# Performance work log

Hardware: AMD Instinct MI355X
Metric: run time of the kernel (lower is better)

Reference implementation:

```python
import jax, jax.numpy as jnp
import numpy as np

R, K, H_IN, W_IN = 512, 17, 56, 56   # rois, keypoints, heatmap size
ROI_H = ROI_W = 96                   # = ceil(BOX_LEN), fixed by construction
BOX_LEN = 95.5                       # all boxes have this side length
A = -0.75                            # PyTorch bicubic coefficient


def _cubic(x):
    x = jnp.abs(x)
    near = ((A + 2.0) * x - (A + 3.0)) * x * x + 1.0
    far = A * (((x - 5.0) * x + 8.0) * x - 4.0)
    return jnp.where(x <= 1.0, near, jnp.where(x < 2.0, far, 0.0))


def _resize_matrix(out_size, in_size):
    """Dense [out,in] bicubic interpolation matrix (align_corners=False, border-replicate)."""
    scale = in_size / out_size
    src = (jnp.arange(out_size, dtype=jnp.float32) + 0.5) * scale - 0.5
    base = jnp.floor(src).astype(jnp.int32)
    taps = base[:, None] + jnp.arange(-1, 3)                      # [out, 4]
    w = _cubic(src[:, None] - taps.astype(jnp.float32))           # weights from unclamped dist
    taps = jnp.clip(taps, 0, in_size - 1)                         # replicate border
    rows = jnp.broadcast_to(jnp.arange(out_size)[:, None], taps.shape)
    return jnp.zeros((out_size, in_size), jnp.float32).at[rows, taps].add(w)


def setup_inputs() -> dict:
    key = jax.random.key(0)
    k1, k2 = jax.random.split(key)
    masks = jax.random.normal(k1, (R, K, H_IN, W_IN), dtype=jnp.float32)
    offs = jax.random.uniform(k2, (R, 2), jnp.float32, 0.0, 400.0)
    # corner format (c0_start, c1_start, c0_end, c1_end); all lengths == BOX_LEN
    boxes = jnp.concatenate([offs, offs + BOX_LEN], axis=1)
    return {"masks": masks, "boxes": boxes}


def reference(masks, boxes):
    My = _resize_matrix(ROI_H, H_IN)   # [ROI_H, H_IN]
    Mx = _resize_matrix(ROI_W, W_IN)   # [ROI_W, W_IN]
    # separable bicubic resize of every ROI heatmap: [R,K,ROI_H,ROI_W]
    roi = jnp.einsum('hi,rkij,wj->rkhw', My, masks, Mx)
    flat = roi.reshape(R, K, ROI_H * ROI_W)
    pos = jnp.argmax(flat, axis=-1)                                # [R,K]
    y = pos // ROI_W
    x = pos % ROI_W
    scores = jnp.take_along_axis(flat, pos[..., None], axis=-1)[..., 0]  # logit at argmax
    len0 = jnp.maximum(boxes[:, 2] - boxes[:, 0], 1.0)
    len1 = jnp.maximum(boxes[:, 3] - boxes[:, 1], 1.0)
    corr0 = (len0 / ROI_H)[:, None]
    corr1 = (len1 / ROI_W)[:, None]
    p0 = (y.astype(jnp.float32) + 0.5) * corr0 + boxes[:, 0:1]
    p1 = (x.astype(jnp.float32) + 0.5) * corr1 + boxes[:, 1:2]
    predictions = jnp.stack([p0, p1, jnp.ones_like(p0)], axis=1)   # [R, n_dim+1, K]
    return predictions, scores
```

## Files before the change

### kernel.cpp

```cpp
#include <hip/hip_runtime.h>

#define R_    512
#define K_    17
#define HIN   56
#define WIN   56
#define OUTS  96
#define NMAP  (R_ * K_)
#define NT    192
#define TS    98
#define TROWS 32

typedef float v2f __attribute__((ext_vector_type(2)));

constexpr float cubic_c(float xin) {
    float x = xin < 0.0f ? -xin : xin;
    const float A = -0.75f;
    if (x <= 1.0f) return ((A + 2.0f) * x - (A + 3.0f)) * x * x + 1.0f;
    if (x < 2.0f)  return A * (((x - 5.0f) * x + 8.0f) * x - 4.0f);
    return 0.0f;
}

struct XTabT {
    float w[OUTS][4];
    int   s[OUTS];
    constexpr XTabT() : w{}, s{} {
        for (int o = 0; o < OUTS; ++o) {
            float src = ((float)o + 0.5f) * (56.0f / 96.0f) - 0.5f;
            int base = (int)src;
            if ((float)base > src) --base;
            int st = base - 1;
            if (st < 0) st = 0;
            if (st > HIN - 4) st = HIN - 4;
            s[o] = st;
            for (int q = 0; q < 4; ++q) {
                int tap = base - 1 + q;
                float wt = cubic_c(src - (float)tap);
                int p = tap < 0 ? 0 : (tap > HIN - 1 ? HIN - 1 : tap);
                w[o][p - st] += wt;
            }
        }
    }
};
constexpr XTabT XT;

struct YTabT {
    float w[12][4];
    int   d[12];
    constexpr YTabT() : w{}, d{} {
        for (int ph = 0; ph < 12; ++ph) {
            float src = ((float)ph + 0.5f) * (56.0f / 96.0f) - 0.5f;
            int base = (int)src;
            if ((float)base > src) --base;
            d[ph] = base - 1;
            for (int q = 0; q < 4; ++q)
                w[ph][q] = cubic_c(src - (float)(base - 1 + q));
        }
    }
};
constexpr YTabT YT;

template<int G>
__device__ __forceinline__ void p1_row(const float* __restrict__ gsrc, float out[32]) {
    constexpr int FS = (G == 0) ? 0 : (G == 1) ? 4 : 9;
    constexpr int NF = (G == 1) ? 6 : 5;
    float r[NF * 4];
    const float4* g4 = (const float4*)gsrc + FS;
#pragma unroll
    for (int i = 0; i < NF; ++i) {
        float4 v = g4[i];
        r[4*i+0] = v.x; r[4*i+1] = v.y; r[4*i+2] = v.z; r[4*i+3] = v.w;
    }
#pragma unroll
    for (int oo = 0; oo < 32; ++oo) {
        const int o  = 32 * G + oo;
        const int rs = XT.s[o] - 4 * FS;
        out[oo] = fmaf(XT.w[o][3], r[rs+3], fmaf(XT.w[o][2], r[rs+2],
                  fmaf(XT.w[o][1], r[rs+1], XT.w[o][0] * r[rs])));
    }
}

__device__ __forceinline__ void p1_phase(const float* __restrict__ masks, float* tbase,
                                         int t, int bm0, int j0, bool lowhalf) {
    const int g = t >> 6;
    const int w = t & 63;
    if (w >= 60) return;
    const int mi = w / 30;
    const int jr = w - 30 * mi;
    const int j  = j0 + jr;
    const float* gsrc = masks + (size_t)(bm0 + mi) * (HIN * WIN) + j * WIN;
    float out[32];
    if      (g == 0) p1_row<0>(gsrc, out);
    else if (g == 1) p1_row<1>(gsrc, out);
    else             p1_row<2>(gsrc, out);
    const int phys = lowhalf ? jr + 2 : jr;
    float* dst = tbase + mi * (TROWS * TS) + phys * TS + 32 * g;
#pragma unroll
    for (int i = 0; i < 16; ++i) ((v2f*)dst)[i] = (v2f){out[2*i], out[2*i+1]};
    if (lowhalf && jr == 0) {
        float* d0 = tbase + mi * (TROWS * TS) + 32 * g;
#pragma unroll
        for (int i = 0; i < 16; ++i) {
            v2f v = (v2f){out[2*i], out[2*i+1]};
            ((v2f*)d0)[i] = v;
            ((v2f*)(d0 + TS))[i] = v;
        }
    }
    if (!lowhalf && jr == 29) {
        float* d0 = tbase + mi * (TROWS * TS) + 30 * TS + 32 * g;
#pragma unroll
        for (int i = 0; i < 16; ++i) {
            v2f v = (v2f){out[2*i], out[2*i+1]};
            ((v2f*)d0)[i] = v;
            ((v2f*)(d0 + TS))[i] = v;
        }
    }
}

__device__ __forceinline__ void p2_block(const float* __restrict__ base, int h0,
                                         float& bx, int& hx, float& by, int& hy) {
    v2f c[18];
#pragma unroll
    for (int i = 0; i < 18; ++i) c[i] = *(const v2f*)(base + i * TS);
#pragma unroll
    for (int hh = 0; hh < 24; ++hh) {
        const int ph = hh % 12;
        const int b  = hh / 12;
        const int i0 = 7 * b + YT.d[ph] + 2;
        const v2f w0 = {YT.w[ph][0], YT.w[ph][0]};
        const v2f w1 = {YT.w[ph][1], YT.w[ph][1]};
        const v2f w2 = {YT.w[ph][2], YT.w[ph][2]};
        const v2f w3 = {YT.w[ph][3], YT.w[ph][3]};
        v2f acc = c[i0] * w0;
        acc = __builtin_elementwise_fma(w1, c[i0+1], acc);
        acc = __builtin_elementwise_fma(w2, c[i0+2], acc);
        acc = __builtin_elementwise_fma(w3, c[i0+3], acc);
        const int h = h0 + hh;
        bool gx = acc.x > bx; bx = gx ? acc.x : bx; hx = gx ? h : hx;
        bool gy = acc.y > by; by = gy ? acc.y : by; hy = gy ? h : hy;
    }
}

__global__ __launch_bounds__(NT)
void _Keypointer_kernel(const float* __restrict__ masks,
                        const float* __restrict__ boxes,
                        float* __restrict__ out) {
    __shared__ float tmp[2 * TROWS * TS];
    __shared__ float redv[NT];
    __shared__ int   redp[NT];

    const int t   = threadIdx.x;
    const int bm0 = 2 * blockIdx.x;

    p1_phase(masks, tmp, t, bm0, 0, true);
    __syncthreads();

    const int mi = t / 96;
    const int v  = t - 96 * mi;
    const int qq = v / 48;
    const int p  = v - 48 * qq;
    const float* pbase = tmp + mi * (TROWS * TS) + (14 * qq) * TS + 2 * p;

    float bx = -INFINITY, by = -INFINITY;
    int hx = 0, hy = 0;
    p2_block(pbase, 24 * qq, bx, hx, by, hy);
    __syncthreads();

    p1_phase(masks, tmp, t, bm0, 26, false);
    __syncthreads();

    p2_block(pbase, 48 + 24 * qq, bx, hx, by, hy);

    int fx = hx * OUTS + 2 * p;
    int fy = hy * OUTS + 2 * p + 1;
    if (by > bx || (by == bx && fy < fx)) { bx = by; fx = fy; }
    redv[t] = bx; redp[t] = fx;
    __syncthreads();

    if (t < 64) {
        const int m = t >> 5, i = t & 31;
        const int b0 = m * 96 + i;
        float bv = redv[b0]; int bp = redp[b0];
#pragma unroll
        for (int o = 32; o < 96; o += 32) {
            float vv = redv[b0 + o]; int pp = redp[b0 + o];
            if (vv > bv || (vv == bv && pp < bp)) { bv = vv; bp = pp; }
        }
#pragma unroll
        for (int off = 16; off > 0; off >>= 1) {
            float vv = __shfl_down(bv, off, 32);
            int   pp = __shfl_down(bp, off, 32);
            if (vv > bv || (vv == bv && pp < bp)) { bv = vv; bp = pp; }
        }
        if (i == 0) {
            const int map = bm0 + m;
            const int r = map / K_, k = map - r * K_;
            const int y = bp / OUTS, x = bp - y * OUTS;
            const float b0f = boxes[r * 4 + 0], b1f = boxes[r * 4 + 1];
            const float b2f = boxes[r * 4 + 2], b3f = boxes[r * 4 + 3];
            const float corr0 = fmaxf(b2f - b0f, 1.0f) / (float)OUTS;
            const float corr1 = fmaxf(b3f - b1f, 1.0f) / (float)OUTS;
            const float p0 = ((float)y + 0.5f) * corr0 + b0f;
            const float p1 = ((float)x + 0.5f) * corr1 + b1f;
            out[(r * 3 + 0) * K_ + k] = p0;
            out[(r * 3 + 1) * K_ + k] = p1;
            out[(r * 3 + 2) * K_ + k] = 1.0f;
            out[R_ * 3 * K_ + r * K_ + k] = bv;
        }
    }
}

extern "C" void kernel_launch(void* const* d_in, const int* in_sizes, int n_in,
                              void* d_out, int out_size, void* d_ws, size_t ws_size,
                              hipStream_t stream) {
    const float* masks = (const float*)d_in[0];
    const float* boxes = (const float*)d_in[1];
    float* out = (float*)d_out;
    _Keypointer_kernel<<<NMAP / 2, NT, 0, stream>>>(masks, boxes, out);
}
```

Baseline: 161.2 us.

## Interleave two maps in shared memory and use max-then-recompute argmax

The horizontal pass now processes the same row of both heatmaps together as v2f pairs. The full 60-row interleaved intermediate is written to shared memory in a single phase, which replaces the two-phase half-tile scheme and its extra barriers. The argmax becomes a value-only max reduction through wave shuffles, after which only threads holding the maximum recompute their column to find the smallest index via atomicMin. This removes the per-element index tracking and the LDS reduction arrays, at the cost of more registers (32 v2f per thread) and a second vertical pass on the winning threads.

```diff
diff --git a/kernel.cpp b/kernel.cpp
--- a/kernel.cpp
+++ b/kernel.cpp
@@ -7,8 +7,8 @@
 #define OUTS  96
 #define NMAP  (R_ * K_)
 #define NT    192
-#define TS    98
-#define TROWS 32
+#define RST   98
+#define TROWS 60
 
 typedef float v2f __attribute__((ext_vector_type(2)));
 
@@ -60,152 +60,129 @@
 constexpr YTabT YT;
 
 template<int G>
-__device__ __forceinline__ void p1_row(const float* __restrict__ gsrc, float out[32]) {
+__device__ __forceinline__ void p1_cols(const float* __restrict__ r0,
+                                        const float* __restrict__ r1,
+                                        v2f* __restrict__ dst) {
     constexpr int FS = (G == 0) ? 0 : (G == 1) ? 4 : 9;
     constexpr int NF = (G == 1) ? 6 : 5;
-    float r[NF * 4];
-    const float4* g4 = (const float4*)gsrc + FS;
+    v2f rr[NF * 4];
+    const float4* A = (const float4*)r0 + FS;
+    const float4* B = (const float4*)r1 + FS;
 #pragma unroll
     for (int i = 0; i < NF; ++i) {
-        float4 v = g4[i];
-        r[4*i+0] = v.x; r[4*i+1] = v.y; r[4*i+2] = v.z; r[4*i+3] = v.w;
+        float4 a = A[i], b = B[i];
+        rr[4 * i + 0] = (v2f){a.x, b.x};
+        rr[4 * i + 1] = (v2f){a.y, b.y};
+        rr[4 * i + 2] = (v2f){a.z, b.z};
+        rr[4 * i + 3] = (v2f){a.w, b.w};
     }
 #pragma unroll
-    for (int oo = 0; oo < 32; ++oo) {
-        const int o  = 32 * G + oo;
-        const int rs = XT.s[o] - 4 * FS;
-        out[oo] = fmaf(XT.w[o][3], r[rs+3], fmaf(XT.w[o][2], r[rs+2],
-                  fmaf(XT.w[o][1], r[rs+1], XT.w[o][0] * r[rs])));
+    for (int i = 0; i < 16; ++i) {
+        const int o0 = 32 * G + 2 * i, o1 = o0 + 1;
+        const int s0 = XT.s[o0] - 4 * FS, s1 = XT.s[o1] - 4 * FS;
+        v2f a0 = rr[s0] * (v2f){XT.w[o0][0], XT.w[o0][0]};
+        a0 = __builtin_elementwise_fma((v2f){XT.w[o0][1], XT.w[o0][1]}, rr[s0 + 1], a0);
+        a0 = __builtin_elementwise_fma((v2f){XT.w[o0][2], XT.w[o0][2]}, rr[s0 + 2], a0);
+        a0 = __builtin_elementwise_fma((v2f){XT.w[o0][3], XT.w[o0][3]}, rr[s0 + 3], a0);
+        v2f a1 = rr[s1] * (v2f){XT.w[o1][0], XT.w[o1][0]};
+        a1 = __builtin_elementwise_fma((v2f){XT.w[o1][1], XT.w[o1][1]}, rr[s1 + 1], a1);
+        a1 = __builtin_elementwise_fma((v2f){XT.w[o1][2], XT.w[o1][2]}, rr[s1 + 2], a1);
+        a1 = __builtin_elementwise_fma((v2f){XT.w[o1][3], XT.w[o1][3]}, rr[s1 + 3], a1);
+        float4 st = {a0.x, a0.y, a1.x, a1.y};
+        *(float4*)(dst + 2 * i) = st;
     }
 }
 
-__device__ __forceinline__ void p1_phase(const float* __restrict__ masks, float* tbase,
-                                         int t, int bm0, int j0, bool lowhalf) {
-    const int g = t >> 6;
-    const int w = t & 63;
-    if (w >= 60) return;
-    const int mi = w / 30;
-    const int jr = w - 30 * mi;
-    const int j  = j0 + jr;
-    const float* gsrc = masks + (size_t)(bm0 + mi) * (HIN * WIN) + j * WIN;
-    float out[32];
-    if      (g == 0) p1_row<0>(gsrc, out);
-    else if (g == 1) p1_row<1>(gsrc, out);
-    else             p1_row<2>(gsrc, out);
-    const int phys = lowhalf ? jr + 2 : jr;
-    float* dst = tbase + mi * (TROWS * TS) + phys * TS + 32 * g;
-#pragma unroll
-    for (int i = 0; i < 16; ++i) ((v2f*)dst)[i] = (v2f){out[2*i], out[2*i+1]};
-    if (lowhalf && jr == 0) {
-        float* d0 = tbase + mi * (TROWS * TS) + 32 * g;
-#pragma unroll
-        for (int i = 0; i < 16; ++i) {
-            v2f v = (v2f){out[2*i], out[2*i+1]};
-            ((v2f*)d0)[i] = v;
-            ((v2f*)(d0 + TS))[i] = v;
-        }
-    }
-    if (!lowhalf && jr == 29) {
-        float* d0 = tbase + mi * (TROWS * TS) + 30 * TS + 32 * g;
-#pragma unroll
-        for (int i = 0; i < 16; ++i) {
-            v2f v = (v2f){out[2*i], out[2*i+1]};
-            ((v2f*)d0)[i] = v;
-            ((v2f*)(d0 + TS))[i] = v;
-        }
-    }
-}
-
-__device__ __forceinline__ void p2_block(const float* __restrict__ base, int h0,
-                                         float& bx, int& hx, float& by, int& hy) {
-    v2f c[18];
-#pragma unroll
-    for (int i = 0; i < 18; ++i) c[i] = *(const v2f*)(base + i * TS);
-#pragma unroll
-    for (int hh = 0; hh < 24; ++hh) {
-        const int ph = hh % 12;
-        const int b  = hh / 12;
-        const int i0 = 7 * b + YT.d[ph] + 2;
-        const v2f w0 = {YT.w[ph][0], YT.w[ph][0]};
-        const v2f w1 = {YT.w[ph][1], YT.w[ph][1]};
-        const v2f w2 = {YT.w[ph][2], YT.w[ph][2]};
-        const v2f w3 = {YT.w[ph][3], YT.w[ph][3]};
-        v2f acc = c[i0] * w0;
-        acc = __builtin_elementwise_fma(w1, c[i0+1], acc);
-        acc = __builtin_elementwise_fma(w2, c[i0+2], acc);
-        acc = __builtin_elementwise_fma(w3, c[i0+3], acc);
-        const int h = h0 + hh;
-        bool gx = acc.x > bx; bx = gx ? acc.x : bx; hx = gx ? h : hx;
-        bool gy = acc.y > by; by = gy ? acc.y : by; hy = gy ? h : hy;
-    }
+__device__ __forceinline__ v2f yv(const v2f* __restrict__ c, int hh) {
+    const int ph = hh % 12, b = hh / 12;
+    const int i0 = 7 * b + YT.d[ph] + 2;
+    v2f acc = c[i0] * (v2f){YT.w[ph][0], YT.w[ph][0]};
+    acc = __builtin_elementwise_fma((v2f){YT.w[ph][1], YT.w[ph][1]}, c[i0 + 1], acc);
+    acc = __builtin_elementwise_fma((v2f){YT.w[ph][2], YT.w[ph][2]}, c[i0 + 2], acc);
+    acc = __builtin_elementwise_fma((v2f){YT.w[ph][3], YT.w[ph][3]}, c[i0 + 3], acc);
+    return acc;
 }
 
 __global__ __launch_bounds__(NT)
 void _Keypointer_kernel(const float* __restrict__ masks,
                         const float* __restrict__ boxes,
                         float* __restrict__ out) {
-    __shared__ float tmp[2 * TROWS * TS];
-    __shared__ float redv[NT];
-    __shared__ int   redp[NT];
+    __shared__ __align__(16) v2f tmp[TROWS * RST];
+    __shared__ v2f wmax[3];
+    __shared__ int candp[2];
 
     const int t   = threadIdx.x;
     const int bm0 = 2 * blockIdx.x;
+    const int g   = t >> 6;
+    const int w   = t & 63;
 
-    p1_phase(masks, tmp, t, bm0, 0, true);
+    const int srcrow = min(max(w - 2, 0), HIN - 1);
+    const int phys   = min(w, TROWS - 1);
+    const float* r0 = masks + (size_t)bm0 * (HIN * WIN) + srcrow * WIN;
+    const float* r1 = r0 + HIN * WIN;
+    v2f* dst = tmp + phys * RST + 32 * g;
+    if      (g == 0) p1_cols<0>(r0, r1, dst);
+    else if (g == 1) p1_cols<1>(r0, r1, dst);
+    else             p1_cols<2>(r0, r1, dst);
+
+    if (t == 0) { candp[0] = 0x7fffffff; candp[1] = 0x7fffffff; }
     __syncthreads();
 
-    const int mi = t / 96;
-    const int v  = t - 96 * mi;
-    const int qq = v / 48;
-    const int p  = v - 48 * qq;
-    const float* pbase = tmp + mi * (TROWS * TS) + (14 * qq) * TS + 2 * p;
+    const int half = (t >= 96) ? 1 : 0;
+    const int col  = t - 96 * half;
+    const int h0   = 48 * half;
+    const v2f* cb  = tmp + (28 * half) * RST + col;
+    v2f c[32];
+#pragma unroll
+    for (int i = 0; i < 32; ++i) c[i] = cb[i * RST];
 
-    float bx = -INFINITY, by = -INFINITY;
-    int hx = 0, hy = 0;
-    p2_block(pbase, 24 * qq, bx, hx, by, hy);
+    v2f vmax = {-INFINITY, -INFINITY};
+#pragma unroll
+    for (int hh = 0; hh < 48; ++hh)
+        vmax = __builtin_elementwise_max(vmax, yv(c, hh));
+
+    float m0 = vmax.x, m1 = vmax.y;
+#pragma unroll
+    for (int off = 32; off > 0; off >>= 1) {
+        m0 = fmaxf(m0, __shfl_down(m0, off, 64));
+        m1 = fmaxf(m1, __shfl_down(m1, off, 64));
+    }
+    if (w == 0) wmax[g] = (v2f){m0, m1};
     __syncthreads();
 
-    p1_phase(masks, tmp, t, bm0, 26, false);
+    const float M0 = fmaxf(fmaxf(wmax[0].x, wmax[1].x), wmax[2].x);
+    const float M1 = fmaxf(fmaxf(wmax[0].y, wmax[1].y), wmax[2].y);
+
+    if (vmax.x == M0 || vmax.y == M1) {
+        int c0 = 0x7fffffff, c1 = 0x7fffffff;
+#pragma unroll
+        for (int hh = 0; hh < 48; ++hh) {
+            v2f a = yv(c, hh);
+            int fp = (h0 + hh) * OUTS + col;
+            if (a.x == M0) c0 = min(c0, fp);
+            if (a.y == M1) c1 = min(c1, fp);
+        }
+        if (c0 != 0x7fffffff) atomicMin(&candp[0], c0);
+        if (c1 != 0x7fffffff) atomicMin(&candp[1], c1);
+    }
     __syncthreads();
 
-    p2_block(pbase, 48 + 24 * qq, bx, hx, by, hy);
-
-    int fx = hx * OUTS + 2 * p;
-    int fy = hy * OUTS + 2 * p + 1;
-    if (by > bx || (by == bx && fy < fx)) { bx = by; fx = fy; }
-    redv[t] = bx; redp[t] = fx;
-    __syncthreads();
-
-    if (t < 64) {
-        const int m = t >> 5, i = t & 31;
-        const int b0 = m * 96 + i;
-        float bv = redv[b0]; int bp = redp[b0];
-#pragma unroll
-        for (int o = 32; o < 96; o += 32) {
-            float vv = redv[b0 + o]; int pp = redp[b0 + o];
-            if (vv > bv || (vv == bv && pp < bp)) { bv = vv; bp = pp; }
-        }
-#pragma unroll
-        for (int off = 16; off > 0; off >>= 1) {
-            float vv = __shfl_down(bv, off, 32);
-            int   pp = __shfl_down(bp, off, 32);
-            if (vv > bv || (vv == bv && pp < bp)) { bv = vv; bp = pp; }
-        }
-        if (i == 0) {
-            const int map = bm0 + m;
-            const int r = map / K_, k = map - r * K_;
-            const int y = bp / OUTS, x = bp - y * OUTS;
-            const float b0f = boxes[r * 4 + 0], b1f = boxes[r * 4 + 1];
-            const float b2f = boxes[r * 4 + 2], b3f = boxes[r * 4 + 3];
-            const float corr0 = fmaxf(b2f - b0f, 1.0f) / (float)OUTS;
-            const float corr1 = fmaxf(b3f - b1f, 1.0f) / (float)OUTS;
-            const float p0 = ((float)y + 0.5f) * corr0 + b0f;
-            const float p1 = ((float)x + 0.5f) * corr1 + b1f;
-            out[(r * 3 + 0) * K_ + k] = p0;
-            out[(r * 3 + 1) * K_ + k] = p1;
-            out[(r * 3 + 2) * K_ + k] = 1.0f;
-            out[R_ * 3 * K_ + r * K_ + k] = bv;
-        }
+    if (t < 2) {
+        const int map = bm0 + t;
+        const float M = t ? M1 : M0;
+        const int bp  = candp[t];
+        const int r = map / K_, k = map - r * K_;
+        const int y = bp / OUTS, x = bp - y * OUTS;
+        const float b0f = boxes[r * 4 + 0], b1f = boxes[r * 4 + 1];
+        const float b2f = boxes[r * 4 + 2], b3f = boxes[r * 4 + 3];
+        const float corr0 = fmaxf(b2f - b0f, 1.0f) / (float)OUTS;
+        const float corr1 = fmaxf(b3f - b1f, 1.0f) / (float)OUTS;
+        const float p0 = ((float)y + 0.5f) * corr0 + b0f;
+        const float p1 = ((float)x + 0.5f) * corr1 + b1f;
+        out[(r * 3 + 0) * K_ + k] = p0;
+        out[(r * 3 + 1) * K_ + k] = p1;
+        out[(r * 3 + 2) * K_ + k] = 1.0f;
+        out[R_ * 3 * K_ + r * K_ + k] = M;
     }
 }
 
```

Result: no change. 158.3 us (-1.8%).
